# Optimization experiments

Hardware: AMD Instinct MI355X
Metric: run time of the kernel (lower is better)

## Reference

```python
import jax, jax.numpy as jnp
import numpy as np

N_NODES = 50000
N_EDGES = 600000
N_GRAPHS = 256
D = 128
D_OUT = 32
NEG_SLOPE = 0.01
EPS = 1e-12


def setup_inputs() -> dict:
    key = jax.random.key(0)
    ks = jax.random.split(key, 10)
    x = jax.random.normal(ks[0], (N_NODES, D), dtype=jnp.float32)
    edge_index = jax.random.randint(ks[1], (2, N_EDGES), 0, N_NODES, dtype=jnp.int64)
    batch = jnp.sort(jax.random.randint(ks[2], (N_NODES,), 0, N_GRAPHS, dtype=jnp.int64))
    s = 1.0 / np.sqrt(D)
    return {
        "x": x,
        "edge_index": edge_index,
        "batch": batch,
        "W_fc1": jax.random.normal(ks[3], (D, D), dtype=jnp.float32) * s,
        "b_fc1": jnp.zeros((D,), dtype=jnp.float32),
        "W_gc1": jax.random.normal(ks[4], (D, D), dtype=jnp.float32) * s,
        "b_gc1": jnp.zeros((D,), dtype=jnp.float32),
        "W_gc2": jax.random.normal(ks[5], (D, D), dtype=jnp.float32) * s,
        "b_gc2": jnp.zeros((D,), dtype=jnp.float32),
        "W_fc2": jax.random.normal(ks[6], (D, D), dtype=jnp.float32) * s,
        "b_fc2": jnp.zeros((D,), dtype=jnp.float32),
        "W_fc3": jax.random.normal(ks[7], (D, D_OUT), dtype=jnp.float32) * s,
        "b_fc3": jnp.zeros((D_OUT,), dtype=jnp.float32),
    }


def _gcn_conv(h, src, dst, inv_sqrt_deg, inv_deg, W, b, n_nodes):
    # GCNConv with self-loops: out = D^{-1/2} (A+I) D^{-1/2} (h @ W) + b
    ht = h @ W  # [N, D]
    coef = inv_sqrt_deg[src] * inv_sqrt_deg[dst]  # [E]
    agg = jax.ops.segment_sum(ht[src] * coef[:, None], dst, num_segments=n_nodes)
    agg = agg + ht * inv_deg[:, None]  # self-loop term
    return agg + b


def reference(x, edge_index, batch, W_fc1, b_fc1, W_gc1, b_gc1, W_gc2, b_gc2,
              W_fc2, b_fc2, W_fc3, b_fc3):
    n = x.shape[0]
    src, dst = edge_index[0], edge_index[1]
    # degree with self-loops (in-degree over targets, unit edge weights)
    deg = jax.ops.segment_sum(jnp.ones_like(dst, dtype=x.dtype), dst, num_segments=n) + 1.0
    inv_sqrt_deg = jax.lax.rsqrt(deg)
    inv_deg = 1.0 / deg

    hx = x @ W_fc1 + b_fc1
    hx = jax.nn.leaky_relu(_gcn_conv(hx, src, dst, inv_sqrt_deg, inv_deg, W_gc1, b_gc1, n), NEG_SLOPE)
    hx = jax.nn.leaky_relu(_gcn_conv(hx, src, dst, inv_sqrt_deg, inv_deg, W_gc2, b_gc2, n), NEG_SLOPE)

    # global mean pool over graphs
    sums = jax.ops.segment_sum(hx, batch, num_segments=N_GRAPHS)  # [G, D]
    counts = jax.ops.segment_sum(jnp.ones((n,), dtype=x.dtype), batch, num_segments=N_GRAPHS)
    pooled = sums / jnp.maximum(counts, 1.0)[:, None]

    # L2 normalize (torch.nn.functional.normalize, p=2, dim=1)
    norm = jnp.sqrt(jnp.sum(pooled * pooled, axis=1, keepdims=True))
    hg = pooled / jnp.maximum(norm, EPS)

    h = jax.nn.leaky_relu(hg @ W_fc2 + b_fc2, NEG_SLOPE)
    out = h @ W_fc3 + b_fc3  # [G, D_OUT]
    return out
```

## Files before the change

kernel.cpp:

```cpp
#include <hip/hip_runtime.h>

#define N_NODES  50000
#define N_EDGES  600000
#define N_GRAPHS 256
#define DOUT     32
#define NEG      0.01f
#define SLOTS    64
#define PSLOTS   16
#define OSLOTS   48
#define GB_GEMM  391
#define NFILL    2048
#define EPB      2344
#define DRANGE   6250

typedef __attribute__((ext_vector_type(8))) short short8;
typedef __attribute__((ext_vector_type(4))) float f32x4;

__device__ __forceinline__ unsigned short bf16_rne(float x) {
    unsigned int u = __float_as_uint(x);
    return (unsigned short)((u + 0x7FFFu + ((u >> 16) & 1u)) >> 16);
}


__global__ __launch_bounds__(256) void k_pre(const float* __restrict__ W1,
                                             const float* __restrict__ b1,
                                             const float* __restrict__ W2,
                                             float* __restrict__ W12,
                                             float* __restrict__ b12,
                                             int* __restrict__ counts,
                                             const int* __restrict__ batch,
                                             int* __restrict__ gs,
                                             int* __restrict__ ge) {
    int bid = blockIdx.x;
    int tid = threadIdx.x;
    if (bid < 65) {
        int i = bid * 2 + (tid >> 7);
        int j = tid & 127;
        if (i < 129) {
            const float* left = (i < 128) ? (W1 + i * 128) : b1;
            float acc = 0.f;
#pragma unroll 4
            for (int k = 0; k < 128; ++k) acc += left[k] * W2[k * 128 + j];
            if (i < 128) W12[i * 128 + j] = acc;
            else b12[j] = acc;
        }
    } else if (bid < 261) {
        int i = (bid - 65) * 256 + tid;
        if (i < N_NODES) counts[i] = 0;
    } else {
        int i = (bid - 261) * 256 + tid;
        if (i < N_NODES) {
            int b = batch[i];
            if (i == 0 || batch[i - 1] != b) gs[b] = i;
            if (i == N_NODES - 1 || batch[i + 1] != b) ge[b] = i + 1;
        }
    }
}


__global__ __launch_bounds__(256) void k_fill_gemm(
    const int* __restrict__ src, const int* __restrict__ dst,
    int* __restrict__ counts, int* __restrict__ csrp, int* __restrict__ csro,
    const float* __restrict__ Xf, const float* __restrict__ Wsrc,
    const float* __restrict__ bias, unsigned short* __restrict__ Y, int n)
{
    __shared__ short Wl[16384];
    int bid = blockIdx.x;
    int tid = threadIdx.x;

    if (bid >= GB_GEMM) {
        int g = bid & 7;
        int first = GB_GEMM + (((g - GB_GEMM) % 8) + 8) % 8;
        int r = (bid - first) >> 3;
        int lo = g * DRANGE, hi = lo + DRANGE;
        int e0 = r * EPB;
        int eend = e0 + EPB; if (eend > N_EDGES) eend = N_EDGES;
#pragma unroll 2
        for (int i = 0; i < 10; ++i) {
            int e = e0 + i * 256 + tid;
            if (e < eend) {
                int d = dst[e];
                if (d >= lo && d < hi) {
                    int s = src[e];
                    int slot = atomicAdd(&counts[d], 1);
                    if (slot < PSLOTS) csrp[(d << 4) + slot] = s;
                    else if (slot < SLOTS) csro[d * OSLOTS + slot - PSLOTS] = s;
                }
            }
        }
        return;
    }

    for (int idx = tid; idx < 16384; idx += 256) {
        float w = Wsrc[idx];
        int k = idx >> 7, c = idx & 127;
        int kt = k >> 5, nt = c >> 4;
        int lane = ((k & 31) >> 3) * 16 + (c & 15);
        int e = k & 7;
        Wl[((kt * 8 + nt) * 64 + lane) * 8 + e] = (short)bf16_rne(w);
    }
    __syncthreads();

    int wid = tid >> 6;
    int lane = tid & 63;
    int r0 = bid * 128 + wid * 32;
    int a0 = r0 + (lane & 15);      if (a0 >= n) a0 = n - 1;
    int a1 = r0 + 16 + (lane & 15); if (a1 >= n) a1 = n - 1;
    int ko = (lane >> 4) * 8;

    f32x4 acc0[8], acc1[8];
    f32x4 zero = {0.f, 0.f, 0.f, 0.f};
#pragma unroll
    for (int t = 0; t < 8; ++t) { acc0[t] = zero; acc1[t] = zero; }

#pragma unroll
    for (int kt = 0; kt < 4; ++kt) {
        int k0 = kt * 32 + ko;
        const float* p0 = Xf + (size_t)a0 * 128 + k0;
        const float* p1 = Xf + (size_t)a1 * 128 + k0;
        float4 u0 = *(const float4*)p0, u1 = *(const float4*)(p0 + 4);
        float4 v0 = *(const float4*)p1, v1 = *(const float4*)(p1 + 4);
        float us[8] = {u0.x, u0.y, u0.z, u0.w, u1.x, u1.y, u1.z, u1.w};
        float vs[8] = {v0.x, v0.y, v0.z, v0.w, v1.x, v1.y, v1.z, v1.w};
        short8 af0, af1;
#pragma unroll
        for (int i = 0; i < 8; ++i) {
            af0[i] = (short)bf16_rne(us[i]);
            af1[i] = (short)bf16_rne(vs[i]);
        }
#pragma unroll
        for (int t = 0; t < 8; ++t) {
            short8 bh = *(const short8*)&Wl[((kt * 8 + t) * 64 + lane) * 8];
            acc0[t] = __builtin_amdgcn_mfma_f32_16x16x32_bf16(af0, bh, acc0[t], 0, 0, 0);
            acc1[t] = __builtin_amdgcn_mfma_f32_16x16x32_bf16(af1, bh, acc1[t], 0, 0, 0);
        }
    }

    int rbase = r0 + (lane >> 4) * 4;
    int col0 = lane & 15;
#pragma unroll
    for (int t = 0; t < 8; ++t) {
        int col = t * 16 + col0;
        float badd = bias[col];
#pragma unroll
        for (int r = 0; r < 4; ++r) {
            int row0 = rbase + r;
            int row1 = rbase + 16 + r;
            if (row0 < n) Y[(size_t)row0 * 128 + col] = bf16_rne(acc0[t][r] + badd);
            if (row1 < n) Y[(size_t)row1 * 128 + col] = bf16_rne(acc1[t][r] + badd);
        }
    }
}


__global__ __launch_bounds__(256) void k_gemm_mfma(
    const unsigned short* __restrict__ Xh, const float* __restrict__ Wsrc,
    unsigned short* __restrict__ Y, int n)
{
    __shared__ short Wl[16384];
    int tid = threadIdx.x;
    for (int idx = tid; idx < 16384; idx += 256) {
        float w = Wsrc[idx];
        int k = idx >> 7, c = idx & 127;
        int kt = k >> 5, nt = c >> 4;
        int lane = ((k & 31) >> 3) * 16 + (c & 15);
        int e = k & 7;
        Wl[((kt * 8 + nt) * 64 + lane) * 8 + e] = (short)bf16_rne(w);
    }
    __syncthreads();

    int wid = tid >> 6;
    int lane = tid & 63;
    int r0 = blockIdx.x * 128 + wid * 32;
    int a0 = r0 + (lane & 15);      if (a0 >= n) a0 = n - 1;
    int a1 = r0 + 16 + (lane & 15); if (a1 >= n) a1 = n - 1;
    int ko = (lane >> 4) * 8;

    f32x4 acc0[8], acc1[8];
    f32x4 zero = {0.f, 0.f, 0.f, 0.f};
#pragma unroll
    for (int t = 0; t < 8; ++t) { acc0[t] = zero; acc1[t] = zero; }

#pragma unroll
    for (int kt = 0; kt < 4; ++kt) {
        int k0 = kt * 32 + ko;
        short8 af0 = *(const short8*)(Xh + (size_t)a0 * 128 + k0);
        short8 af1 = *(const short8*)(Xh + (size_t)a1 * 128 + k0);
#pragma unroll
        for (int t = 0; t < 8; ++t) {
            short8 bh = *(const short8*)&Wl[((kt * 8 + t) * 64 + lane) * 8];
            acc0[t] = __builtin_amdgcn_mfma_f32_16x16x32_bf16(af0, bh, acc0[t], 0, 0, 0);
            acc1[t] = __builtin_amdgcn_mfma_f32_16x16x32_bf16(af1, bh, acc1[t], 0, 0, 0);
        }
    }

    int rbase = r0 + (lane >> 4) * 4;
    int col0 = lane & 15;
#pragma unroll
    for (int t = 0; t < 8; ++t) {
        int col = t * 16 + col0;
#pragma unroll
        for (int r = 0; r < 4; ++r) {
            int row0 = rbase + r;
            int row1 = rbase + 16 + r;
            if (row0 < n) Y[(size_t)row0 * 128 + col] = bf16_rne(acc0[t][r]);
            if (row1 < n) Y[(size_t)row1 * 128 + col] = bf16_rne(acc1[t][r]);
        }
    }
}


__global__ __launch_bounds__(256) void k_agg(const unsigned short* __restrict__ HT,
                                             const int* __restrict__ csrp,
                                             const int* __restrict__ csro,
                                             const int* __restrict__ counts,
                                             const float* __restrict__ bias,
                                             unsigned short* __restrict__ OUT, int n) {
    int node = blockIdx.x * 4 + (threadIdx.x >> 6);
    int lane = threadIdx.x & 63;
    if (node >= n) return;
    const unsigned int* H = (const unsigned int*)HT;
    int deg = counts[node];
    float is = rsqrtf((float)deg + 1.0f);
    int c1 = deg < PSLOTS ? deg : PSLOTS;
    int base = node << 4;

    unsigned int su = H[(size_t)node * 64 + lane];
    float2 b = ((const float2*)bias)[lane];

    float acc0 = 0.f, acc1 = 0.f, acc2 = 0.f, acc3 = 0.f;
    int j = 0;
    for (; j + 8 <= c1; j += 8) {
        int sx[8];
#pragma unroll
        for (int q = 0; q < 8; ++q) sx[q] = csrp[base + j + q];
        int dg[8];
#pragma unroll
        for (int q = 0; q < 8; ++q) dg[q] = counts[sx[q]];
        unsigned int v[8];
#pragma unroll
        for (int q = 0; q < 8; ++q) v[q] = H[(size_t)sx[q] * 64 + lane];
#pragma unroll
        for (int q = 0; q < 8; ++q) {
            float c = rsqrtf((float)dg[q] + 1.0f) * is;
            float f0 = __uint_as_float(v[q] << 16);
            float f1 = __uint_as_float(v[q] & 0xFFFF0000u);
            if (q & 1) { acc2 += f0 * c; acc3 += f1 * c; }
            else       { acc0 += f0 * c; acc1 += f1 * c; }
        }
    }
    for (; j + 4 <= c1; j += 4) {
        int sx[4];
#pragma unroll
        for (int q = 0; q < 4; ++q) sx[q] = csrp[base + j + q];
        int dg[4];
#pragma unroll
        for (int q = 0; q < 4; ++q) dg[q] = counts[sx[q]];
        unsigned int v[4];
#pragma unroll
        for (int q = 0; q < 4; ++q) v[q] = H[(size_t)sx[q] * 64 + lane];
#pragma unroll
        for (int q = 0; q < 4; ++q) {
            float c = rsqrtf((float)dg[q] + 1.0f) * is;
            float f0 = __uint_as_float(v[q] << 16);
            float f1 = __uint_as_float(v[q] & 0xFFFF0000u);
            if (q & 1) { acc2 += f0 * c; acc3 += f1 * c; }
            else       { acc0 += f0 * c; acc1 += f1 * c; }
        }
    }
    for (; j < c1; ++j) {
        int s = csrp[base + j];
        float c = rsqrtf((float)counts[s] + 1.0f) * is;
        unsigned int v = H[(size_t)s * 64 + lane];
        acc0 += __uint_as_float(v << 16) * c;
        acc1 += __uint_as_float(v & 0xFFFF0000u) * c;
    }
    int c2 = deg < SLOTS ? deg : SLOTS;
    for (j = PSLOTS; j < c2; ++j) {
        int s = csro[node * OSLOTS + j - PSLOTS];
        float c = rsqrtf((float)counts[s] + 1.0f) * is;
        unsigned int v = H[(size_t)s * 64 + lane];
        acc0 += __uint_as_float(v << 16) * c;
        acc1 += __uint_as_float(v & 0xFFFF0000u) * c;
    }

    float invd = is * is;
    float sv0 = __uint_as_float(su << 16);
    float sv1 = __uint_as_float(su & 0xFFFF0000u);
    float ox = acc0 + acc2 + sv0 * invd + b.x;
    float oy = acc1 + acc3 + sv1 * invd + b.y;
    ox = ox > 0.f ? ox : ox * NEG;
    oy = oy > 0.f ? oy : oy * NEG;
    unsigned int pk = (unsigned int)bf16_rne(ox) | ((unsigned int)bf16_rne(oy) << 16);
    ((unsigned int*)OUT)[(size_t)node * 64 + lane] = pk;
}


__global__ __launch_bounds__(256) void k_pool_final(const unsigned short* __restrict__ Hn,
                                                    const int* __restrict__ gs,
                                                    const int* __restrict__ ge,
                                                    const float* __restrict__ W2,
                                                    const float* __restrict__ b2,
                                                    const float* __restrict__ W3,
                                                    const float* __restrict__ b3,
                                                    float* __restrict__ out) {
    __shared__ float part[4][128];
    __shared__ float red[128];
    __shared__ float h1[128];
    int g = blockIdx.x, tid = threadIdx.x;
    int c2 = tid & 63, rr = tid >> 6;
    int s = gs[g], e = ge[g];
    const unsigned int* H = (const unsigned int*)Hn;
    float2 acc = make_float2(0.f, 0.f);
    for (int r = s + rr; r < e; r += 4) {
        unsigned int v = H[(size_t)r * 64 + c2];
        acc.x += __uint_as_float(v << 16);
        acc.y += __uint_as_float(v & 0xFFFF0000u);
    }
    part[rr][c2 * 2] = acc.x;
    part[rr][c2 * 2 + 1] = acc.y;
    __syncthreads();
    float mean = 0.f;
    if (tid < 128) {
        mean = (part[0][tid] + part[1][tid] + part[2][tid] + part[3][tid])
               / fmaxf((float)(e - s), 1.f);
        red[tid] = mean * mean;
    }
    __syncthreads();
    for (int off = 64; off > 0; off >>= 1) {
        if (tid < off) red[tid] += red[tid + off];
        __syncthreads();
    }
    if (tid < 128) {
        float norm = sqrtf(red[0]);
        part[0][tid] = mean / fmaxf(norm, 1e-12f);
    }
    __syncthreads();
    if (tid < 128) {
        float a = b2[tid];
#pragma unroll 8
        for (int k = 0; k < 128; ++k) a += part[0][k] * W2[k * 128 + tid];
        a = a > 0.f ? a : a * NEG;
        h1[tid] = a;
    }
    __syncthreads();
    if (tid < DOUT) {
        float a2 = b3[tid];
#pragma unroll 8
        for (int k = 0; k < 128; ++k) a2 += h1[k] * W3[k * DOUT + tid];
        out[g * DOUT + tid] = a2;
    }
}


extern "C" void kernel_launch(void* const* d_in, const int* in_sizes, int n_in,
                              void* d_out, int out_size, void* d_ws, size_t ws_size,
                              hipStream_t stream) {
    const float* x      = (const float*)d_in[0];
    const int*   ei     = (const int*)d_in[1];
    const int*   batch  = (const int*)d_in[2];
    const float* W_fc1  = (const float*)d_in[3];
    const float* b_fc1  = (const float*)d_in[4];
    const float* W_gc1  = (const float*)d_in[5];
    const float* b_gc1  = (const float*)d_in[6];
    const float* W_gc2  = (const float*)d_in[7];
    const float* b_gc2  = (const float*)d_in[8];
    const float* W_fc2  = (const float*)d_in[9];
    const float* b_fc2  = (const float*)d_in[10];
    const float* W_fc3  = (const float*)d_in[11];
    const float* b_fc3  = (const float*)d_in[12];
    float* out = (float*)d_out;

    const int N = N_NODES, E = N_EDGES;
    const int* e_src = ei;
    const int* e_dst = ei + E;

    char* ws = (char*)d_ws;
    unsigned short* H0     = (unsigned short*)(ws + 0);
    unsigned short* H1     = (unsigned short*)(ws + 12800000);
    int*            csrp   = (int*)  (ws + 25600000);
    int*            csro   = (int*)  (ws + 28800000);
    int*            counts = (int*)  (ws + 38400000);
    int*            gs     = (int*)  (ws + 38600000);
    int*            ge     = (int*)  (ws + 38601024);
    float*          W12    = (float*)(ws + 38602048);
    float*          b12    = (float*)(ws + 38667584);

    k_pre<<<457, 256, 0, stream>>>(W_fc1, b_fc1, W_gc1, W12, b12, counts, batch, gs, ge);
    k_fill_gemm<<<GB_GEMM + NFILL, 256, 0, stream>>>(e_src, e_dst, counts, csrp, csro,
                                                     x, W12, b12, H1, N);
    k_agg<<<(N + 3) / 4, 256, 0, stream>>>(H1, csrp, csro, counts, b_gc1, H0, N);
    k_gemm_mfma<<<GB_GEMM, 256, 0, stream>>>(H0, W_gc2, H1, N);
    k_agg<<<(N + 3) / 4, 256, 0, stream>>>(H1, csrp, csro, counts, b_gc2, H0, N);
    k_pool_final<<<N_GRAPHS, 256, 0, stream>>>(H0, gs, ge, W_fc2, b_fc2, W_fc3, b_fc3, out);

    (void)in_sizes; (void)n_in; (void)out_size; (void)ws_size;
}
```

Measured before the change: 161.0 us.

## Use XCC-aware dynamic chunk queues for CSR fill instead of static block mapping

```diff
diff --git a/kernel.cpp b/kernel.cpp
--- a/kernel.cpp
+++ b/kernel.cpp
@@ -9,8 +9,9 @@
 #define PSLOTS   16
 #define OSLOTS   48
 #define GB_GEMM  391
-#define NFILL    2048
-#define EPB      2344
+#define NFILLQ   1024
+#define CHUNK    2048
+#define NCHUNK   293
 #define DRANGE   6250
 
 typedef __attribute__((ext_vector_type(8))) short short8;
@@ -46,7 +47,7 @@
         }
     } else if (bid < 261) {
         int i = (bid - 65) * 256 + tid;
-        if (i < N_NODES) counts[i] = 0;
+        if (i < N_NODES + 8) counts[i] = 0;
     } else {
         int i = (bid - 261) * 256 + tid;
         if (i < N_NODES) {
@@ -60,7 +61,8 @@
 
 __global__ __launch_bounds__(256) void k_fill_gemm(
     const int* __restrict__ src, const int* __restrict__ dst,
-    int* __restrict__ counts, int* __restrict__ csrp, int* __restrict__ csro,
+    int* __restrict__ counts, int* __restrict__ qhead,
+    int* __restrict__ csrp, int* __restrict__ csro,
     const float* __restrict__ Xf, const float* __restrict__ Wsrc,
     const float* __restrict__ bias, unsigned short* __restrict__ Y, int n)
 {
@@ -69,22 +71,32 @@
     int tid = threadIdx.x;
 
     if (bid >= GB_GEMM) {
-        int g = bid & 7;
-        int first = GB_GEMM + (((g - GB_GEMM) % 8) + 8) % 8;
-        int r = (bid - first) >> 3;
-        int lo = g * DRANGE, hi = lo + DRANGE;
-        int e0 = r * EPB;
-        int eend = e0 + EPB; if (eend > N_EDGES) eend = N_EDGES;
-#pragma unroll 2
-        for (int i = 0; i < 10; ++i) {
-            int e = e0 + i * 256 + tid;
-            if (e < eend) {
-                int d = dst[e];
-                if (d >= lo && d < hi) {
-                    int s = src[e];
-                    int slot = atomicAdd(&counts[d], 1);
-                    if (slot < PSLOTS) csrp[(d << 4) + slot] = s;
-                    else if (slot < SLOTS) csro[d * OSLOTS + slot - PSLOTS] = s;
+        __shared__ int c_sh;
+        int g0;
+        asm volatile("s_getreg_b32 %0, hwreg(HW_REG_XCC_ID)" : "=s"(g0));
+        g0 &= 7;
+        for (int pass = 0; pass < 8; ++pass) {
+            int g = (g0 + pass) & 7;
+            int lo = g * DRANGE, hi = lo + DRANGE;
+            for (;;) {
+                __syncthreads();
+                if (tid == 0) c_sh = atomicAdd(&qhead[g], 1);
+                __syncthreads();
+                int c = c_sh;
+                if (c >= NCHUNK) break;
+                int e0 = c * CHUNK;
+#pragma unroll
+                for (int i = 0; i < CHUNK / 256; ++i) {
+                    int e = e0 + i * 256 + tid;
+                    if (e < N_EDGES) {
+                        int d = dst[e];
+                        if (d >= lo && d < hi) {
+                            int s = src[e];
+                            int slot = atomicAdd(&counts[d], 1);
+                            if (slot < PSLOTS) csrp[(d << 4) + slot] = s;
+                            else if (slot < SLOTS) csro[d * OSLOTS + slot - PSLOTS] = s;
+                        }
+                    }
                 }
             }
         }
@@ -371,9 +383,9 @@
     const float* b_fc3  = (const float*)d_in[12];
     float* out = (float*)d_out;
 
-    const int N = N_NODES, E = N_EDGES;
+    const int N = N_NODES;
     const int* e_src = ei;
-    const int* e_dst = ei + E;
+    const int* e_dst = ei + N_EDGES;
 
     char* ws = (char*)d_ws;
     unsigned short* H0     = (unsigned short*)(ws + 0);
@@ -381,14 +393,15 @@
     int*            csrp   = (int*)  (ws + 25600000);
     int*            csro   = (int*)  (ws + 28800000);
     int*            counts = (int*)  (ws + 38400000);
-    int*            gs     = (int*)  (ws + 38600000);
-    int*            ge     = (int*)  (ws + 38601024);
-    float*          W12    = (float*)(ws + 38602048);
-    float*          b12    = (float*)(ws + 38667584);
+    int*            qhead  = (int*)  (ws + 38600000);
+    int*            gs     = (int*)  (ws + 38601024);
+    int*            ge     = (int*)  (ws + 38602048);
+    float*          W12    = (float*)(ws + 38603072);
+    float*          b12    = (float*)(ws + 38668608);
 
     k_pre<<<457, 256, 0, stream>>>(W_fc1, b_fc1, W_gc1, W12, b12, counts, batch, gs, ge);
-    k_fill_gemm<<<GB_GEMM + NFILL, 256, 0, stream>>>(e_src, e_dst, counts, csrp, csro,
-                                                     x, W12, b12, H1, N);
+    k_fill_gemm<<<GB_GEMM + NFILLQ, 256, 0, stream>>>(e_src, e_dst, counts, qhead,
+                                                      csrp, csro, x, W12, b12, H1, N);
     k_agg<<<(N + 3) / 4, 256, 0, stream>>>(H1, csrp, csro, counts, b_gc1, H0, N);
     k_gemm_mfma<<<GB_GEMM, 256, 0, stream>>>(H0, W_gc2, H1, N);
     k_agg<<<(N + 3) / 4, 256, 0, stream>>>(H1, csrp, csro, counts, b_gc2, H0, N);
```

Measured after the change: 253.3 us. +57.3%, slower.
